# Performance work log

Hardware: AMD Instinct MI355X
Metric: run time of the kernel (lower is better)

Reference implementation:

```python
import jax, jax.numpy as jnp
import numpy as np

N_NODES = 100000
N_EDGES = 1600000


def setup_inputs() -> dict:
    key = jax.random.key(0)
    ks = jax.random.split(key, 5)
    x = jax.random.normal(ks[0], (N_NODES, 128), dtype=jnp.float32)
    edge_index = jax.random.randint(ks[1], (2, N_EDGES), 0, N_NODES, dtype=jnp.int64)
    edge_weight = jnp.ones((N_EDGES,), dtype=jnp.float32)
    W1 = jax.random.normal(ks[2], (128, 128), dtype=jnp.float32) * (1.0 / np.sqrt(128))
    b1 = jnp.zeros((128,), dtype=jnp.float32)
    W2 = jax.random.normal(ks[3], (128, 64), dtype=jnp.float32) * (1.0 / np.sqrt(128))
    b2 = jnp.zeros((64,), dtype=jnp.float32)
    return {"x": x, "edge_index": edge_index, "edge_weight": edge_weight,
            "W1": W1, "b1": b1, "W2": W2, "b2": b2}


def _gcn_conv(x, rows, cols, W, b, n_nodes):
    # GCNConv(normalize=True), unit edge weights (forward overwrites weights with ones)
    h = x @ W                                             # [N, out]
    ones_w = jnp.ones(rows.shape[0], dtype=x.dtype)
    deg = jax.ops.segment_sum(ones_w, cols, num_segments=n_nodes)   # in-degree at targets
    dinv = jnp.where(deg > 0, deg ** -0.5, 0.0)
    norm = dinv[rows] * dinv[cols]                        # [E+N]
    msg = h[rows] * norm[:, None]                         # gather + scale, memory-bound
    out = jax.ops.segment_sum(msg, cols, num_segments=n_nodes)
    return out + b


def reference(x, edge_index, edge_weight, W1, b1, W2, b2):
    n = x.shape[0]
    loop = jnp.arange(n, dtype=edge_index.dtype)
    rows = jnp.concatenate([edge_index[0], loop])         # self-loops (PyG default)
    cols = jnp.concatenate([edge_index[1], loop])
    h = jax.nn.relu(_gcn_conv(x, rows, cols, W1, b1, n))
    logits = _gcn_conv(h, rows, cols, W2, b2, n)
    return logits
```

## Files before the change

kernel.cpp:

```cpp
#include <hip/hip_runtime.h>
#include <hip/hip_fp16.h>


constexpr int NN = 100000;
constexpr int NE = 1600000;
constexpr int BSH = 7;
constexpr int NB = (NN + 127) >> BSH;
constexpr int NBLK = 256;
constexpr int EPB = NE / NBLK;
constexpr int TSTR = 784;

typedef _Float16 f16x8 __attribute__((ext_vector_type(8)));
typedef float f32x4 __attribute__((ext_vector_type(4)));

__global__ __launch_bounds__(256) void k_hist(const int* __restrict__ cols,
                                              int* __restrict__ table) {
  __shared__ int cnt[NB];
  for (int i = threadIdx.x; i < NB; i += 256) cnt[i] = 0;
  __syncthreads();
  int base = blockIdx.x * EPB;
  for (int i = threadIdx.x; i < EPB; i += 256)
    atomicAdd(&cnt[cols[base + i] >> BSH], 1);
  __syncthreads();
  for (int i = threadIdx.x; i < NB; i += 256)
    table[blockIdx.x * TSTR + i] = cnt[i];
}

__global__ __launch_bounds__(256) void k_scanT(const int* __restrict__ table,
                                               int* __restrict__ startOff,
                                               int* __restrict__ btot) {
  __shared__ int s[256];
  int b = blockIdx.x, t = threadIdx.x;
  int v = table[t * TSTR + b];
  s[t] = v;
  __syncthreads();
  for (int off = 1; off < 256; off <<= 1) {
    int tmp = (t >= off) ? s[t - off] : 0;
    __syncthreads();
    s[t] += tmp;
    __syncthreads();
  }
  startOff[t * TSTR + b] = s[t] - v;
  if (t == 255) btot[b] = s[t];
}

__global__ __launch_bounds__(256) void k_scanBkt(const int* __restrict__ btot,
                                                 int* __restrict__ bucketBase) {
  __shared__ int s[256];
  int t = threadIdx.x;
  int base = t * 4;
  int d0 = (base + 0 < NB) ? btot[base + 0] : 0;
  int d1 = (base + 1 < NB) ? btot[base + 1] : 0;
  int d2 = (base + 2 < NB) ? btot[base + 2] : 0;
  int d3 = (base + 3 < NB) ? btot[base + 3] : 0;
  int tsum = d0 + d1 + d2 + d3;
  s[t] = tsum;
  __syncthreads();
  for (int off = 1; off < 256; off <<= 1) {
    int tmp = (t >= off) ? s[t - off] : 0;
    __syncthreads();
    s[t] += tmp;
    __syncthreads();
  }
  int ex = s[t] - tsum;
  if (base + 0 < NB) bucketBase[base + 0] = ex;
  if (base + 1 < NB) bucketBase[base + 1] = ex + d0;
  if (base + 2 < NB) bucketBase[base + 2] = ex + d0 + d1;
  if (base + 3 < NB) bucketBase[base + 3] = ex + d0 + d1 + d2;
}

__global__ __launch_bounds__(256) void k_scat(const int* __restrict__ rows,
                                              const int* __restrict__ cols,
                                              const int* __restrict__ startOff,
                                              const int* __restrict__ bucketBase,
                                              unsigned* __restrict__ binned) {
  __shared__ int scnt[NB];
  int blk = blockIdx.x;
  for (int i = threadIdx.x; i < NB; i += 256)
    scnt[i] = bucketBase[i] + startOff[blk * TSTR + i];
  __syncthreads();
  int base = blk * EPB;
  for (int i = threadIdx.x; i < EPB; i += 256) {
    int c = cols[base + i];
    int r = rows[base + i];
    int pos = atomicAdd(&scnt[c >> BSH], 1);
    binned[pos] = ((unsigned)r << BSH) | (unsigned)(c & 127);
  }
}

__global__ __launch_bounds__(256) void k_fillb(const unsigned* __restrict__ binned,
                                               const int* __restrict__ bucketBase,
                                               const int* __restrict__ btot,
                                               const float4* __restrict__ x4,
                                               int* __restrict__ rowptr,
                                               int* __restrict__ deg,
                                               float* __restrict__ dinv,
                                               int* __restrict__ srcIdx,
                                               float2* __restrict__ y8) {
  __shared__ int cnt[128];
  __shared__ int sc[128];
  __shared__ int rp[128];
  __shared__ float dnv[128];
  int b = blockIdx.x;
  int nb0 = b << BSH;
  int nn = min(128, NN - nb0);
  int tid = threadIdx.x;
  if (tid < 128) cnt[tid] = 0;
  __syncthreads();
  int ebeg = bucketBase[b];
  int eend = ebeg + btot[b];
  for (int p = ebeg + tid; p < eend; p += 256)
    atomicAdd(&cnt[binned[p] & 127], 1);
  __syncthreads();
  int v = (tid < 128) ? cnt[tid] : 0;
  if (tid < 128) sc[tid] = v;
  __syncthreads();
  for (int off = 1; off < 128; off <<= 1) {
    int tmp = (tid < 128 && tid >= off) ? sc[tid - off] : 0;
    __syncthreads();
    if (tid < 128) sc[tid] += tmp;
    __syncthreads();
  }
  if (tid < 128) {
    int ex = sc[tid] - v;
    rp[tid] = ebeg + ex;
    float dv = rsqrtf((float)v + 1.0f);
    dnv[tid] = dv;
    if (tid < nn) {
      rowptr[nb0 + tid] = ebeg + ex;
      deg[nb0 + tid] = v;
      dinv[nb0 + tid] = dv;
    }
    cnt[tid] = 0;
  }
  __syncthreads();
  for (int p = ebeg + tid; p < eend; p += 256) {
    unsigned pk = binned[p];
    int cl = pk & 127;
    int local = atomicAdd(&cnt[cl], 1);
    srcIdx[rp[cl] + local] = (int)(pk >> BSH);
  }
  for (int i = tid; i < nn * 32; i += 256) {
    int n = i >> 5, j = i & 31;
    float s = dnv[n];
    float4 vv = x4[(size_t)(nb0 + n) * 32 + j];
    union { __half2 h[2]; float2 f; } u;
    u.h[0] = __floats2half2_rn(vv.x * s, vv.y * s);
    u.h[1] = __floats2half2_rn(vv.z * s, vv.w * s);
    y8[(size_t)(nb0 + n) * 32 + j] = u.f;
  }
}

__global__ __launch_bounds__(256) void k_wt(const float* __restrict__ W1,
                                            const float* __restrict__ W2,
                                            __half* __restrict__ Wt1,
                                            __half* __restrict__ Wt2) {
  int i = blockIdx.x * 256 + threadIdx.x;
  if (i < 128 * 128) {
    int k = i >> 7, n = i & 127;
    Wt1[n * 128 + k] = __float2half(W1[i]);
  } else if (i < 128 * 128 + 128 * 64) {
    int j = i - 128 * 128;
    int k = j >> 6, n = j & 63;
    Wt2[n * 128 + k] = __float2half(W2[j]);
  }
}

__global__ __launch_bounds__(256) void k_gath1(const __half2* __restrict__ y2,
                                               const int* __restrict__ rowptr,
                                               const int* __restrict__ deg,
                                               const int* __restrict__ srcIdx,
                                               const float* __restrict__ dinv,
                                               __half2* __restrict__ agg) {
  int node = blockIdx.x * 4 + (threadIdx.x >> 6);
  int lane = threadIdx.x & 63;
  int g = lane >> 4, m = lane & 15;
  int d = deg[node];
  int p = rowptr[node];
  float acc[8];
#pragma unroll
  for (int j = 0; j < 8; j++) acc[j] = 0.0f;

  for (int base = 0; base < d; base += 64) {
    int cnt = min(64, d - base);
    int my = srcIdx[min(p + base + lane, NE - 1)];
    int k = 0;
    for (; k + 8 <= cnt; k += 8) {
      int s0 = __shfl(my, k + g);
      int s1 = __shfl(my, k + 4 + g);
      float4 f0 = *reinterpret_cast<const float4*>(y2 + (size_t)s0 * 64 + m * 4);
      float4 f1 = *reinterpret_cast<const float4*>(y2 + (size_t)s1 * 64 + m * 4);
      const __half2* h0 = reinterpret_cast<const __half2*>(&f0);
      const __half2* h1 = reinterpret_cast<const __half2*>(&f1);
#pragma unroll
      for (int q = 0; q < 4; q++) {
        float2 a = __half22float2(h0[q]);
        float2 bb = __half22float2(h1[q]);
        acc[2 * q] += a.x + bb.x;
        acc[2 * q + 1] += a.y + bb.y;
      }
    }
    for (; k < cnt; k += 4) {
      int e = k + g;
      int s0 = __shfl(my, min(e, cnt - 1));
      if (e < cnt) {
        float4 f0 = *reinterpret_cast<const float4*>(y2 + (size_t)s0 * 64 + m * 4);
        const __half2* h0 = reinterpret_cast<const __half2*>(&f0);
#pragma unroll
        for (int q = 0; q < 4; q++) {
          float2 a = __half22float2(h0[q]);
          acc[2 * q] += a.x;
          acc[2 * q + 1] += a.y;
        }
      }
    }
  }
#pragma unroll
  for (int j = 0; j < 8; j++) {
    acc[j] += __shfl_xor(acc[j], 16);
    acc[j] += __shfl_xor(acc[j], 32);
  }
  if (g == 0) {
    float4 fs = *reinterpret_cast<const float4*>(y2 + (size_t)node * 64 + m * 4);
    const __half2* hs = reinterpret_cast<const __half2*>(&fs);
    float sc = dinv[node];
    union { __half2 h[4]; float4 f; } o;
#pragma unroll
    for (int q = 0; q < 4; q++) {
      float2 a = __half22float2(hs[q]);
      o.h[q] = __floats2half2_rn((acc[2 * q] + a.x) * sc, (acc[2 * q + 1] + a.y) * sc);
    }
    *reinterpret_cast<float4*>(agg + (size_t)node * 64 + m * 4) = o.f;
  }
}

__global__ __launch_bounds__(256) void k_gath2(const __half2* __restrict__ z2,
                                               const int* __restrict__ rowptr,
                                               const int* __restrict__ deg,
                                               const int* __restrict__ srcIdx,
                                               const float* __restrict__ dinv,
                                               const float* __restrict__ b2,
                                               float* __restrict__ out) {
  int node = blockIdx.x * 4 + (threadIdx.x >> 6);
  int lane = threadIdx.x & 63;
  int g = lane >> 3, m = lane & 7;
  int d = deg[node];
  int p = rowptr[node];
  float acc[8];
#pragma unroll
  for (int j = 0; j < 8; j++) acc[j] = 0.0f;

  for (int base = 0; base < d; base += 64) {
    int cnt = min(64, d - base);
    int my = srcIdx[min(p + base + lane, NE - 1)];
    int k = 0;
    for (; k + 16 <= cnt; k += 16) {
      int s0 = __shfl(my, k + g);
      int s1 = __shfl(my, k + 8 + g);
      float4 f0 = *reinterpret_cast<const float4*>(z2 + (size_t)s0 * 32 + m * 4);
      float4 f1 = *reinterpret_cast<const float4*>(z2 + (size_t)s1 * 32 + m * 4);
      const __half2* h0 = reinterpret_cast<const __half2*>(&f0);
      const __half2* h1 = reinterpret_cast<const __half2*>(&f1);
#pragma unroll
      for (int q = 0; q < 4; q++) {
        float2 a = __half22float2(h0[q]);
        float2 bb = __half22float2(h1[q]);
        acc[2 * q] += a.x + bb.x;
        acc[2 * q + 1] += a.y + bb.y;
      }
    }
    for (; k < cnt; k += 8) {
      int e = k + g;
      int s0 = __shfl(my, min(e, cnt - 1));
      if (e < cnt) {
        float4 f0 = *reinterpret_cast<const float4*>(z2 + (size_t)s0 * 32 + m * 4);
        const __half2* h0 = reinterpret_cast<const __half2*>(&f0);
#pragma unroll
        for (int q = 0; q < 4; q++) {
          float2 a = __half22float2(h0[q]);
          acc[2 * q] += a.x;
          acc[2 * q + 1] += a.y;
        }
      }
    }
  }
#pragma unroll
  for (int j = 0; j < 8; j++) {
    acc[j] += __shfl_xor(acc[j], 8);
    acc[j] += __shfl_xor(acc[j], 16);
    acc[j] += __shfl_xor(acc[j], 32);
  }
  if (g == 0) {
    float4 fs = *reinterpret_cast<const float4*>(z2 + (size_t)node * 32 + m * 4);
    const __half2* hs = reinterpret_cast<const __half2*>(&fs);
    float s = dinv[node];
    float4 bv0 = *reinterpret_cast<const float4*>(b2 + m * 8);
    float4 bv1 = *reinterpret_cast<const float4*>(b2 + m * 8 + 4);
    float2 a0 = __half22float2(hs[0]), a1 = __half22float2(hs[1]);
    float2 a2 = __half22float2(hs[2]), a3 = __half22float2(hs[3]);
    float4 o0 = make_float4((acc[0] + a0.x) * s + bv0.x, (acc[1] + a0.y) * s + bv0.y,
                            (acc[2] + a1.x) * s + bv0.z, (acc[3] + a1.y) * s + bv0.w);
    float4 o1 = make_float4((acc[4] + a2.x) * s + bv1.x, (acc[5] + a2.y) * s + bv1.y,
                            (acc[6] + a3.x) * s + bv1.z, (acc[7] + a3.y) * s + bv1.w);
    *reinterpret_cast<float4*>(out + (size_t)node * 64 + m * 8) = o0;
    *reinterpret_cast<float4*>(out + (size_t)node * 64 + m * 8 + 4) = o1;
  }
}

template <int BN, bool BIASRELU, bool ROWSCALE>
__global__ __launch_bounds__(256) void k_gemmM(const __half* __restrict__ A,
                                               const __half* __restrict__ Wt,
                                               const float* __restrict__ bias,
                                               const float* __restrict__ rowscale,
                                               __half* __restrict__ C, int M) {
  constexpr int NT = BN / 16;
  __shared__ __half tile[4][16][BN + 8];
  const int w = threadIdx.x >> 6, l = threadIdx.x & 63;
  const int quad = l >> 4, m = l & 15;
  const int rowTop = blockIdx.x * 64 + w * 16;

  f32x4 acc[NT];
#pragma unroll
  for (int t = 0; t < NT; t++) {
    float bv = BIASRELU ? bias[t * 16 + m] : 0.0f;
    acc[t] = (f32x4){bv, bv, bv, bv};
  }

  int arow = rowTop + m;
  if (arow >= M) arow = M - 1;
  const __half* ap = A + (size_t)arow * 128 + quad * 8;

#pragma unroll
  for (int kc = 0; kc < 128; kc += 32) {
    f16x8 a = *reinterpret_cast<const f16x8*>(ap + kc);
#pragma unroll
    for (int t = 0; t < NT; t++) {
      f16x8 b = *reinterpret_cast<const f16x8*>(
          Wt + (size_t)(t * 16 + m) * 128 + kc + quad * 8);
      acc[t] = __builtin_amdgcn_mfma_f32_16x16x32_f16(a, b, acc[t], 0, 0, 0);
    }
  }

  float rs[4];
  if constexpr (ROWSCALE) {
#pragma unroll
    for (int i = 0; i < 4; i++) {
      int r = rowTop + quad * 4 + i;
      rs[i] = rowscale[r < M ? r : M - 1];
    }
  }
#pragma unroll
  for (int t = 0; t < NT; t++)
#pragma unroll
    for (int i = 0; i < 4; i++) {
      float v = acc[t][i];
      if constexpr (BIASRELU) v = fmaxf(v, 0.0f);
      if constexpr (ROWSCALE) v *= rs[i];
      tile[w][quad * 4 + i][t * 16 + m] = __float2half(v);
    }
  __syncthreads();

  constexpr int CH = 16 * BN / 8;
#pragma unroll
  for (int rep = 0; rep < CH / 64; rep++) {
    int idx = rep * 64 + l;
    int r = idx / (BN / 8), cc = idx % (BN / 8);
    int grow = rowTop + r;
    if (grow < M)
      *reinterpret_cast<float4*>(C + (size_t)grow * BN + cc * 8) =
          *reinterpret_cast<const float4*>(&tile[w][r][cc * 8]);
  }
}

extern "C" void kernel_launch(void* const* d_in, const int* in_sizes, int n_in,
                              void* d_out, int out_size, void* d_ws, size_t ws_size,
                              hipStream_t stream) {
  const float* x  = (const float*)d_in[0];
  const int*   ei = (const int*)d_in[1];
  const int* rows = ei;
  const int* cols = ei + NE;
  const float* W1 = (const float*)d_in[3];
  const float* b1 = (const float*)d_in[4];
  const float* W2 = (const float*)d_in[5];
  const float* b2 = (const float*)d_in[6];
  float* out = (float*)d_out;

  char* base = (char*)d_ws;
  constexpr size_t MB = 1 << 20;
  int*      deg       = (int*)(base + 0 * MB);
  int*      rowptr    = (int*)(base + 1 * MB);
  float*    dinv      = (float*)(base + 2 * MB);
  int*      btot      = (int*)(base + 3 * MB);
  int*      bucketBase= (int*)(base + 3 * MB + 16 * 1024);
  __half*   Wt1       = (__half*)(base + 3 * MB + 64 * 1024);
  __half*   Wt2       = (__half*)(base + 3 * MB + 128 * 1024);
  int*      table     = (int*)(base + 4 * MB);
  int*      startOff  = (int*)(base + 5 * MB);
  unsigned* binned    = (unsigned*)(base + 6 * MB);
  int*      srcIdx    = (int*)(base + 13 * MB);
  __half2*  y         = (__half2*)(base + 20 * MB);
  __half*   aggx      = (__half*)(base + 46 * MB);
  __half*   h1        = (__half*)(base + 72 * MB);
  __half2*  z         = (__half2*)(base + 20 * MB);

  k_wt<<<96, 256, 0, stream>>>(W1, W2, Wt1, Wt2);
  k_hist<<<NBLK, 256, 0, stream>>>(cols, table);
  k_scanT<<<NB, 256, 0, stream>>>(table, startOff, btot);
  k_scanBkt<<<1, 256, 0, stream>>>(btot, bucketBase);
  k_scat<<<NBLK, 256, 0, stream>>>(rows, cols, startOff, bucketBase, binned);
  k_fillb<<<NB, 256, 0, stream>>>(binned, bucketBase, btot, (const float4*)x,
                                  rowptr, deg, dinv, srcIdx, (float2*)y);
  k_gath1<<<NN / 4, 256, 0, stream>>>(y, rowptr, deg, srcIdx, dinv,
                                      (__half2*)aggx);
  k_gemmM<128, true, false><<<(NN + 63) / 64, 256, 0, stream>>>(
      aggx, Wt1, b1, nullptr, h1, NN);
  k_gemmM<64, false, true><<<(NN + 63) / 64, 256, 0, stream>>>(
      h1, Wt2, nullptr, dinv, (__half*)z, NN);
  k_gath2<<<NN / 4, 256, 0, stream>>>(z, rowptr, deg, srcIdx, dinv, b2, out);
}
```

Baseline: 331.3 us.

## Fuse fp16 conversion into histogram and apply source scaling inside gather

Converts x to fp16 and transposes the weights inside the histogram kernel, removing the separate weight kernel and the dinv-scaled feature write in fillb. The first gather now loads dinv per source edge and scales on the fly, and both gathers unroll more loads per iteration. The scatter kernel uses half as many blocks, each handling two histogram slices. This adds per-edge dinv lookups and more register pressure in exchange for fewer kernels and less serial work in fillb.

```diff
diff --git a/kernel.cpp b/kernel.cpp
--- a/kernel.cpp
+++ b/kernel.cpp
@@ -14,16 +14,39 @@
 typedef float f32x4 __attribute__((ext_vector_type(4)));
 
 __global__ __launch_bounds__(256) void k_hist(const int* __restrict__ cols,
-                                              int* __restrict__ table) {
+                                              int* __restrict__ table,
+                                              const float4* __restrict__ x4,
+                                              float2* __restrict__ xh2,
+                                              const float* __restrict__ W1,
+                                              const float* __restrict__ W2,
+                                              __half* __restrict__ Wt1,
+                                              __half* __restrict__ Wt2) {
   __shared__ int cnt[NB];
   for (int i = threadIdx.x; i < NB; i += 256) cnt[i] = 0;
   __syncthreads();
-  int base = blockIdx.x * EPB;
+  int blk = blockIdx.x;
+  int wi = blk * 256 + (int)threadIdx.x;
+  if (wi < 128 * 128) {
+    int k = wi >> 7, n = wi & 127;
+    Wt1[n * 128 + k] = __float2half(W1[wi]);
+  } else if (wi < 128 * 128 + 128 * 64) {
+    int j = wi - 128 * 128;
+    int k = j >> 6, n = j & 63;
+    Wt2[n * 128 + k] = __float2half(W2[j]);
+  }
+  int base = blk * EPB;
   for (int i = threadIdx.x; i < EPB; i += 256)
     atomicAdd(&cnt[cols[base + i] >> BSH], 1);
+  for (int i = blk * 256 + (int)threadIdx.x; i < NN * 32; i += 256 * NBLK) {
+    float4 v = x4[i];
+    union { __half2 h[2]; float2 f; } u;
+    u.h[0] = __floats2half2_rn(v.x, v.y);
+    u.h[1] = __floats2half2_rn(v.z, v.w);
+    xh2[i] = u.f;
+  }
   __syncthreads();
   for (int i = threadIdx.x; i < NB; i += 256)
-    table[blockIdx.x * TSTR + i] = cnt[i];
+    table[blk * TSTR + i] = cnt[i];
 }
 
 __global__ __launch_bounds__(256) void k_scanT(const int* __restrict__ table,
@@ -77,10 +100,10 @@
   __shared__ int scnt[NB];
   int blk = blockIdx.x;
   for (int i = threadIdx.x; i < NB; i += 256)
-    scnt[i] = bucketBase[i] + startOff[blk * TSTR + i];
-  __syncthreads();
-  int base = blk * EPB;
-  for (int i = threadIdx.x; i < EPB; i += 256) {
+    scnt[i] = bucketBase[i] + startOff[(2 * blk) * TSTR + i];
+  __syncthreads();
+  int base = 2 * blk * EPB;
+  for (int i = threadIdx.x; i < 2 * EPB; i += 256) {
     int c = cols[base + i];
     int r = rows[base + i];
     int pos = atomicAdd(&scnt[c >> BSH], 1);
@@ -91,16 +114,13 @@
 __global__ __launch_bounds__(256) void k_fillb(const unsigned* __restrict__ binned,
                                                const int* __restrict__ bucketBase,
                                                const int* __restrict__ btot,
-                                               const float4* __restrict__ x4,
                                                int* __restrict__ rowptr,
                                                int* __restrict__ deg,
                                                float* __restrict__ dinv,
-                                               int* __restrict__ srcIdx,
-                                               float2* __restrict__ y8) {
+                                               int* __restrict__ srcIdx) {
   __shared__ int cnt[128];
   __shared__ int sc[128];
   __shared__ int rp[128];
-  __shared__ float dnv[128];
   int b = blockIdx.x;
   int nb0 = b << BSH;
   int nn = min(128, NN - nb0);
@@ -124,12 +144,10 @@
   if (tid < 128) {
     int ex = sc[tid] - v;
     rp[tid] = ebeg + ex;
-    float dv = rsqrtf((float)v + 1.0f);
-    dnv[tid] = dv;
     if (tid < nn) {
       rowptr[nb0 + tid] = ebeg + ex;
       deg[nb0 + tid] = v;
-      dinv[nb0 + tid] = dv;
+      dinv[nb0 + tid] = rsqrtf((float)v + 1.0f);
     }
     cnt[tid] = 0;
   }
@@ -140,38 +158,14 @@
     int local = atomicAdd(&cnt[cl], 1);
     srcIdx[rp[cl] + local] = (int)(pk >> BSH);
   }
-  for (int i = tid; i < nn * 32; i += 256) {
-    int n = i >> 5, j = i & 31;
-    float s = dnv[n];
-    float4 vv = x4[(size_t)(nb0 + n) * 32 + j];
-    union { __half2 h[2]; float2 f; } u;
-    u.h[0] = __floats2half2_rn(vv.x * s, vv.y * s);
-    u.h[1] = __floats2half2_rn(vv.z * s, vv.w * s);
-    y8[(size_t)(nb0 + n) * 32 + j] = u.f;
-  }
-}
-
-__global__ __launch_bounds__(256) void k_wt(const float* __restrict__ W1,
-                                            const float* __restrict__ W2,
-                                            __half* __restrict__ Wt1,
-                                            __half* __restrict__ Wt2) {
-  int i = blockIdx.x * 256 + threadIdx.x;
-  if (i < 128 * 128) {
-    int k = i >> 7, n = i & 127;
-    Wt1[n * 128 + k] = __float2half(W1[i]);
-  } else if (i < 128 * 128 + 128 * 64) {
-    int j = i - 128 * 128;
-    int k = j >> 6, n = j & 63;
-    Wt2[n * 128 + k] = __float2half(W2[j]);
-  }
-}
-
-__global__ __launch_bounds__(256) void k_gath1(const __half2* __restrict__ y2,
+}
+
+__global__ __launch_bounds__(256) void k_gath1(const float4* __restrict__ xh4,
                                                const int* __restrict__ rowptr,
                                                const int* __restrict__ deg,
                                                const int* __restrict__ srcIdx,
                                                const float* __restrict__ dinv,
-                                               __half2* __restrict__ agg) {
+                                               float4* __restrict__ agg4) {
   int node = blockIdx.x * 4 + (threadIdx.x >> 6);
   int lane = threadIdx.x & 63;
   int g = lane >> 4, m = lane & 15;
@@ -184,33 +178,42 @@
   for (int base = 0; base < d; base += 64) {
     int cnt = min(64, d - base);
     int my = srcIdx[min(p + base + lane, NE - 1)];
+    float dv = dinv[my];
     int k = 0;
-    for (; k + 8 <= cnt; k += 8) {
-      int s0 = __shfl(my, k + g);
-      int s1 = __shfl(my, k + 4 + g);
-      float4 f0 = *reinterpret_cast<const float4*>(y2 + (size_t)s0 * 64 + m * 4);
-      float4 f1 = *reinterpret_cast<const float4*>(y2 + (size_t)s1 * 64 + m * 4);
+    for (; k + 16 <= cnt; k += 16) {
+      int s0 = __shfl(my, k + g);       float e0 = __shfl(dv, k + g);
+      int s1 = __shfl(my, k + 4 + g);   float e1 = __shfl(dv, k + 4 + g);
+      int s2 = __shfl(my, k + 8 + g);   float e2 = __shfl(dv, k + 8 + g);
+      int s3 = __shfl(my, k + 12 + g);  float e3 = __shfl(dv, k + 12 + g);
+      float4 f0 = xh4[(size_t)s0 * 16 + m];
+      float4 f1 = xh4[(size_t)s1 * 16 + m];
+      float4 f2 = xh4[(size_t)s2 * 16 + m];
+      float4 f3 = xh4[(size_t)s3 * 16 + m];
       const __half2* h0 = reinterpret_cast<const __half2*>(&f0);
       const __half2* h1 = reinterpret_cast<const __half2*>(&f1);
+      const __half2* h2 = reinterpret_cast<const __half2*>(&f2);
+      const __half2* h3 = reinterpret_cast<const __half2*>(&f3);
 #pragma unroll
       for (int q = 0; q < 4; q++) {
-        float2 a = __half22float2(h0[q]);
-        float2 bb = __half22float2(h1[q]);
-        acc[2 * q] += a.x + bb.x;
-        acc[2 * q + 1] += a.y + bb.y;
+        float2 a0 = __half22float2(h0[q]), a1 = __half22float2(h1[q]);
+        float2 a2 = __half22float2(h2[q]), a3 = __half22float2(h3[q]);
+        acc[2 * q]     += e0 * a0.x + e1 * a1.x + e2 * a2.x + e3 * a3.x;
+        acc[2 * q + 1] += e0 * a0.y + e1 * a1.y + e2 * a2.y + e3 * a3.y;
       }
     }
     for (; k < cnt; k += 4) {
       int e = k + g;
-      int s0 = __shfl(my, min(e, cnt - 1));
+      int sel = min(e, cnt - 1);
+      int s0 = __shfl(my, sel);
+      float e0 = __shfl(dv, sel);
       if (e < cnt) {
-        float4 f0 = *reinterpret_cast<const float4*>(y2 + (size_t)s0 * 64 + m * 4);
+        float4 f0 = xh4[(size_t)s0 * 16 + m];
         const __half2* h0 = reinterpret_cast<const __half2*>(&f0);
 #pragma unroll
         for (int q = 0; q < 4; q++) {
-          float2 a = __half22float2(h0[q]);
-          acc[2 * q] += a.x;
-          acc[2 * q + 1] += a.y;
+          float2 a0 = __half22float2(h0[q]);
+          acc[2 * q] += e0 * a0.x;
+          acc[2 * q + 1] += e0 * a0.y;
         }
       }
     }
@@ -221,20 +224,21 @@
     acc[j] += __shfl_xor(acc[j], 32);
   }
   if (g == 0) {
-    float4 fs = *reinterpret_cast<const float4*>(y2 + (size_t)node * 64 + m * 4);
+    float4 fs = xh4[(size_t)node * 16 + m];
     const __half2* hs = reinterpret_cast<const __half2*>(&fs);
-    float sc = dinv[node];
+    float dc = dinv[node];
     union { __half2 h[4]; float4 f; } o;
 #pragma unroll
     for (int q = 0; q < 4; q++) {
       float2 a = __half22float2(hs[q]);
-      o.h[q] = __floats2half2_rn((acc[2 * q] + a.x) * sc, (acc[2 * q + 1] + a.y) * sc);
-    }
-    *reinterpret_cast<float4*>(agg + (size_t)node * 64 + m * 4) = o.f;
-  }
-}
-
-__global__ __launch_bounds__(256) void k_gath2(const __half2* __restrict__ z2,
+      o.h[q] = __floats2half2_rn((acc[2 * q] + dc * a.x) * dc,
+                                 (acc[2 * q + 1] + dc * a.y) * dc);
+    }
+    agg4[(size_t)node * 16 + m] = o.f;
+  }
+}
+
+__global__ __launch_bounds__(256) void k_gath2(const float4* __restrict__ z4,
                                                const int* __restrict__ rowptr,
                                                const int* __restrict__ deg,
                                                const int* __restrict__ srcIdx,
@@ -254,32 +258,39 @@
     int cnt = min(64, d - base);
     int my = srcIdx[min(p + base + lane, NE - 1)];
     int k = 0;
-    for (; k + 16 <= cnt; k += 16) {
+    for (; k + 32 <= cnt; k += 32) {
       int s0 = __shfl(my, k + g);
       int s1 = __shfl(my, k + 8 + g);
-      float4 f0 = *reinterpret_cast<const float4*>(z2 + (size_t)s0 * 32 + m * 4);
-      float4 f1 = *reinterpret_cast<const float4*>(z2 + (size_t)s1 * 32 + m * 4);
+      int s2 = __shfl(my, k + 16 + g);
+      int s3 = __shfl(my, k + 24 + g);
+      float4 f0 = z4[(size_t)s0 * 8 + m];
+      float4 f1 = z4[(size_t)s1 * 8 + m];
+      float4 f2 = z4[(size_t)s2 * 8 + m];
+      float4 f3 = z4[(size_t)s3 * 8 + m];
       const __half2* h0 = reinterpret_cast<const __half2*>(&f0);
       const __half2* h1 = reinterpret_cast<const __half2*>(&f1);
+      const __half2* h2 = reinterpret_cast<const __half2*>(&f2);
+      const __half2* h3 = reinterpret_cast<const __half2*>(&f3);
 #pragma unroll
       for (int q = 0; q < 4; q++) {
-        float2 a = __half22float2(h0[q]);
-        float2 bb = __half22float2(h1[q]);
-        acc[2 * q] += a.x + bb.x;
-        acc[2 * q + 1] += a.y + bb.y;
+        float2 a0 = __half22float2(h0[q]), a1 = __half22float2(h1[q]);
+        float2 a2 = __half22float2(h2[q]), a3 = __half22float2(h3[q]);
+        acc[2 * q]     += (a0.x + a1.x) + (a2.x + a3.x);
+        acc[2 * q + 1] += (a0.y + a1.y) + (a2.y + a3.y);
       }
     }
     for (; k < cnt; k += 8) {
       int e = k + g;
-      int s0 = __shfl(my, min(e, cnt - 1));
+      int sel = min(e, cnt - 1);
+      int s0 = __shfl(my, sel);
       if (e < cnt) {
-        float4 f0 = *reinterpret_cast<const float4*>(z2 + (size_t)s0 * 32 + m * 4);
+        float4 f0 = z4[(size_t)s0 * 8 + m];
         const __half2* h0 = reinterpret_cast<const __half2*>(&f0);
 #pragma unroll
         for (int q = 0; q < 4; q++) {
-          float2 a = __half22float2(h0[q]);
-          acc[2 * q] += a.x;
-          acc[2 * q + 1] += a.y;
+          float2 a0 = __half22float2(h0[q]);
+          acc[2 * q] += a0.x;
+          acc[2 * q + 1] += a0.y;
         }
       }
     }
@@ -291,7 +302,7 @@
     acc[j] += __shfl_xor(acc[j], 32);
   }
   if (g == 0) {
-    float4 fs = *reinterpret_cast<const float4*>(z2 + (size_t)node * 32 + m * 4);
+    float4 fs = z4[(size_t)node * 8 + m];
     const __half2* hs = reinterpret_cast<const __half2*>(&fs);
     float s = dinv[node];
     float4 bv0 = *reinterpret_cast<const float4*>(b2 + m * 8);
@@ -398,23 +409,24 @@
   int*      startOff  = (int*)(base + 5 * MB);
   unsigned* binned    = (unsigned*)(base + 6 * MB);
   int*      srcIdx    = (int*)(base + 13 * MB);
-  __half2*  y         = (__half2*)(base + 20 * MB);
+  __half*   xh        = (__half*)(base + 20 * MB);
   __half*   aggx      = (__half*)(base + 46 * MB);
   __half*   h1        = (__half*)(base + 72 * MB);
-  __half2*  z         = (__half2*)(base + 20 * MB);
-
-  k_wt<<<96, 256, 0, stream>>>(W1, W2, Wt1, Wt2);
-  k_hist<<<NBLK, 256, 0, stream>>>(cols, table);
+  __half*   z         = (__half*)(base + 20 * MB);
+
+  k_hist<<<NBLK, 256, 0, stream>>>(cols, table, (const float4*)x, (float2*)xh,
+                                   W1, W2, Wt1, Wt2);
   k_scanT<<<NB, 256, 0, stream>>>(table, startOff, btot);
   k_scanBkt<<<1, 256, 0, stream>>>(btot, bucketBase);
-  k_scat<<<NBLK, 256, 0, stream>>>(rows, cols, startOff, bucketBase, binned);
-  k_fillb<<<NB, 256, 0, stream>>>(binned, bucketBase, btot, (const float4*)x,
-                                  rowptr, deg, dinv, srcIdx, (float2*)y);
-  k_gath1<<<NN / 4, 256, 0, stream>>>(y, rowptr, deg, srcIdx, dinv,
-                                      (__half2*)aggx);
+  k_scat<<<128, 256, 0, stream>>>(rows, cols, startOff, bucketBase, binned);
+  k_fillb<<<NB, 256, 0, stream>>>(binned, bucketBase, btot, rowptr, deg, dinv,
+                                  srcIdx);
+  k_gath1<<<NN / 4, 256, 0, stream>>>((const float4*)xh, rowptr, deg, srcIdx,
+                                      dinv, (float4*)aggx);
   k_gemmM<128, true, false><<<(NN + 63) / 64, 256, 0, stream>>>(
       aggx, Wt1, b1, nullptr, h1, NN);
   k_gemmM<64, false, true><<<(NN + 63) / 64, 256, 0, stream>>>(
-      h1, Wt2, nullptr, dinv, (__half*)z, NN);
-  k_gath2<<<NN / 4, 256, 0, stream>>>(z, rowptr, deg, srcIdx, dinv, b2, out);
-}
+      h1, Wt2, nullptr, dinv, z, NN);
+  k_gath2<<<NN / 4, 256, 0, stream>>>((const float4*)z, rowptr, deg, srcIdx,
+                                      dinv, b2, out);
+}
```

Result: slower. 358.8 us (+8.3%).
